# Optimization experiments

Hardware: AMD Instinct MI355X
Metric: run time of the kernel (lower is better)

The kernel has to match this reference:

```python
import jax, jax.numpy as jnp
import numpy as np

B, L, D = 16, 64, 768
E, R, T = 100000, 200, 1000000
NUM_WAYS, NUM_STEPS = 2, 3


def setup_inputs() -> dict:
    key = jax.random.key(0)
    k = jax.random.split(key, 12)
    s = 0.02  # matches nn.init.normal_(std=0.02)
    return {
        "heads": jax.random.uniform(k[0], (B, E), dtype=jnp.float32),
        "q_embeddings": jax.random.normal(k[1], (B, D), dtype=jnp.float32),
        "q_word_h": jax.random.normal(k[2], (B, L, D), dtype=jnp.float32),
        "attention_mask": jnp.ones((B, L), dtype=jnp.int32),
        "entity_range": jnp.ones((B, E), dtype=jnp.float32),
        "subj": jax.random.randint(k[3], (T,), 0, E, dtype=jnp.int32),
        "rel": jax.random.randint(k[4], (T,), 0, R, dtype=jnp.int32),
        "obj": jax.random.randint(k[5], (T,), 0, E, dtype=jnp.int32),
        "rel_importance": jnp.ones((R,), dtype=jnp.float32),
        "entity_emb": jax.random.normal(k[6], (E, D), dtype=jnp.float32) * s,
        "match_w": jax.random.normal(k[7], (D, D), dtype=jnp.float32) * s,
        "match_b": jnp.zeros((D,), dtype=jnp.float32),
        "step_w": jax.random.normal(k[8], (NUM_WAYS * NUM_STEPS, D, D), dtype=jnp.float32) * s,
        "step_b": jnp.zeros((NUM_WAYS * NUM_STEPS, D), dtype=jnp.float32),
        "rel_w": jax.random.normal(k[9], (NUM_WAYS, D, R), dtype=jnp.float32) * s,
        "rel_b": jnp.zeros((NUM_WAYS, R), dtype=jnp.float32),
        "hop_w": jax.random.normal(k[10], (NUM_WAYS, D, NUM_STEPS), dtype=jnp.float32) * s,
        "hop_b": jnp.zeros((NUM_WAYS, NUM_STEPS), dtype=jnp.float32),
        "temperature": jnp.ones((1,), dtype=jnp.float32),
    }


def _safe_row_norm(x):
    s = jnp.sum(x, axis=1, keepdims=True)
    return x / jnp.where(s > 0, s, 1.0)


def reference(heads, q_embeddings, q_word_h, attention_mask, entity_range,
              subj, rel, obj, rel_importance, entity_emb, match_w, match_b,
              step_w, step_b, rel_w, rel_b, hop_w, hop_b, temperature):
    # follow(e, r): sparse.mm(Msubj, e.T) is a row-gather e[:, subj];
    # sparse.mm(Mrel, wr.T) is wr[:, rel]; Mobj.T @ x is scatter-add over obj.
    def follow(e, r):
        wr = r * rel_importance[None, :]                      # [B, R]
        x = jnp.take(e, subj, axis=1) * jnp.take(wr, rel, axis=1)  # [B, T]
        res = jnp.zeros_like(e).at[:, obj].add(x)             # [B, E]
        res = jnp.clip(res, 0.0, 1.0)
        m = jnp.max(res, axis=1, keepdims=True)
        return res / jnp.where(m > 0, m, 1.0)

    mask_f = attention_mask.astype(jnp.float32)
    d = q_embeddings.shape[-1]
    # direct entity matching (dropout = identity in eval)
    qem = q_embeddings @ match_w + match_b
    direct = jax.nn.sigmoid((qem @ entity_emb.T) / jnp.sqrt(jnp.float32(d)))
    enhanced = _safe_row_norm(heads * (1.0 + 0.3 * direct))

    e_score = jnp.zeros_like(heads)
    for w in range(NUM_WAYS):
        last_e = enhanced  # num_ways > 1 branch
        ent_probs = []
        for t in range(NUM_STEPS):
            i = w * NUM_STEPS + t
            cq = jnp.tanh(q_embeddings @ step_w[i] + step_b[i])       # [B, D]
            q_logits = jnp.einsum('bd,bld->bl', cq, q_word_h) / temperature
            q_dist = jax.nn.softmax(q_logits, axis=1) * mask_f
            q_dist = q_dist / (jnp.sum(q_dist, axis=1, keepdims=True) + 1e-6)
            ctx = jnp.einsum('bl,bld->bd', q_dist, q_word_h)          # [B, D]
            rel_dist = jax.nn.softmax(ctx @ rel_w[w] + rel_b[w], axis=-1)
            next_e = follow(last_e, rel_dist)
            if t > 0:
                next_e = 0.7 * next_e + 0.3 * last_e  # residual, res_weight=0.3
            last_e = _safe_row_norm(next_e * entity_range)
            ent_probs.append(last_e)
        hop_res = jnp.stack(ent_probs, axis=1)                        # [B, S, E]
        hop_attn = jax.nn.softmax(q_embeddings @ hop_w[w] + hop_b[w], axis=1)[:, :, None]
        way_e = jnp.sum(hop_res * hop_attn, axis=1)                   # [B, E]
        if w == 0:
            way_e = way_e * (1.0 + 0.15 * direct)  # final_direct_weight
        e_score = e_score + way_e
    return e_score
```

## Files before the change

### kernel.cpp

```cpp
#include <hip/hip_runtime.h>
#include <cstdint>

constexpr int kB = 16;
constexpr int kL = 64;
constexpr int kD = 768;
constexpr int kE = 100000;
constexpr int kR = 200;
constexpr int kT = 1000000;
constexpr size_t kEB = (size_t)kE * 16;
constexpr int kEBq = kE * 4;

__global__ void __launch_bounds__(256) k_init(const float* __restrict__ heads,
        const float* __restrict__ er, float* __restrict__ headsT, float* __restrict__ erT,
        float* __restrict__ escT, int* __restrict__ cnt, unsigned* __restrict__ rmax,
        float* __restrict__ ssum, float* __restrict__ hsum) {
    int tid = blockIdx.x * blockDim.x + threadIdx.x;
    int gsz = gridDim.x * blockDim.x;
    if (tid < 96) { rmax[tid] = 0u; ssum[tid] = 0.f; }
    if (tid < 16) hsum[tid] = 0.f;
    float4 z4 = make_float4(0.f, 0.f, 0.f, 0.f);
    float4* esc4 = (float4*)escT;
    for (int i = tid; i < kEBq; i += gsz) esc4[i] = z4;
    for (int i = tid; i < kE; i += gsz) cnt[i] = 0;
    const float4* h4 = (const float4*)heads;
    const float4* r4 = (const float4*)er;
    for (int q = tid; q < kE / 4; q += gsz) {
        float hv[16][4], rv[16][4];
#pragma unroll
        for (int b = 0; b < 16; b++) {
            float4 h = h4[b * (kE / 4) + q];
            float4 r = r4[b * (kE / 4) + q];
            hv[b][0] = h.x; hv[b][1] = h.y; hv[b][2] = h.z; hv[b][3] = h.w;
            rv[b][0] = r.x; rv[b][1] = r.y; rv[b][2] = r.z; rv[b][3] = r.w;
        }
        float4* oh = (float4*)headsT + (size_t)q * 16;
        float4* orr = (float4*)erT + (size_t)q * 16;
#pragma unroll
        for (int u = 0; u < 4; u++) {
#pragma unroll
            for (int c = 0; c < 4; c++) {
                oh[u * 4 + c] = make_float4(hv[4*c][u], hv[4*c+1][u], hv[4*c+2][u], hv[4*c+3][u]);
                orr[u * 4 + c] = make_float4(rv[4*c][u], rv[4*c+1][u], rv[4*c+2][u], rv[4*c+3][u]);
            }
        }
    }
}

__global__ void k_hist(const int* __restrict__ obj, int* __restrict__ cnt) {
    int i = blockIdx.x * blockDim.x + threadIdx.x;
    int st = gridDim.x * blockDim.x;
    for (; i < kT; i += st) atomicAdd(&cnt[obj[i]], 1);
}

__global__ void k_scan1(const int* __restrict__ cnt, int* __restrict__ row, int* __restrict__ bsum) {
    __shared__ int s[512];
    int o = blockIdx.x * 512 + threadIdx.x;
    int v = (o < kE) ? cnt[o] : 0;
    s[threadIdx.x] = v;
    __syncthreads();
    for (int off = 1; off < 512; off <<= 1) {
        int t = (threadIdx.x >= off) ? s[threadIdx.x - off] : 0;
        __syncthreads();
        s[threadIdx.x] += t;
        __syncthreads();
    }
    if (o < kE) row[o + 1] = s[threadIdx.x];
    if (threadIdx.x == 511) bsum[blockIdx.x] = s[511];
}

__global__ void k_scan2(int* __restrict__ bsum, int nb) {
    __shared__ int s[256];
    int t = threadIdx.x;
    int v = (t < nb) ? bsum[t] : 0;
    s[t] = v;
    __syncthreads();
    for (int off = 1; off < 256; off <<= 1) {
        int x = (t >= off) ? s[t - off] : 0;
        __syncthreads();
        s[t] += x;
        __syncthreads();
    }
    if (t < nb) bsum[t] = s[t] - v;
}

__global__ void k_scan3(const int* __restrict__ cnt, int* __restrict__ row,
                        int* __restrict__ fill, const int* __restrict__ bsum) {
    int o = blockIdx.x * blockDim.x + threadIdx.x;
    if (o == 0) row[0] = 0;
    if (o < kE) {
        int incl = row[o + 1] + bsum[o / 512];
        row[o + 1] = incl;
        fill[o] = incl - cnt[o];
    }
}

__global__ void k_scatter(const int* __restrict__ subj, const int* __restrict__ rel,
                          const int* __restrict__ obj, int* __restrict__ fill,
                          int2* __restrict__ sr) {
    int i = blockIdx.x * blockDim.x + threadIdx.x;
    int st = gridDim.x * blockDim.x;
    for (; i < kT; i += st) {
        int o = obj[i];
        int p = atomicAdd(&fill[o], 1);
        sr[p] = make_int2(subj[i], rel[i]);
    }
}

__global__ void __launch_bounds__(192) k_dense(const float* __restrict__ q,
        const float* __restrict__ mw, const float* __restrict__ mb,
        const float* __restrict__ sw, const float* __restrict__ sb,
        float* __restrict__ cq) {
    int tid = threadIdx.x;
    int b = blockIdx.x, i = blockIdx.y;
    const float* W    = (i == 0) ? mw : sw + (size_t)(i - 1) * kD * kD;
    const float* bias = (i == 0) ? mb : sb + (size_t)(i - 1) * kD;
    const float* qr   = q + (size_t)b * kD;
    const float4* W4 = (const float4*)W;
    float4 acc = ((const float4*)bias)[tid];
#pragma unroll 4
    for (int k = 0; k < kD; k++) {
        float qk = qr[k];
        float4 wv = W4[k * 192 + tid];
        acc.x += qk * wv.x; acc.y += qk * wv.y; acc.z += qk * wv.z; acc.w += qk * wv.w;
    }
    if (i > 0) { acc.x = tanhf(acc.x); acc.y = tanhf(acc.y); acc.z = tanhf(acc.z); acc.w = tanhf(acc.w); }
    ((float4*)cq)[((size_t)i * 16 + b) * 192 + tid] = acc;
}

__global__ void __launch_bounds__(192) k_hop(const float* __restrict__ q,
        const float* __restrict__ hw, const float* __restrict__ hb,
        float* __restrict__ hopL) {
    int w = blockIdx.x, b = blockIdx.y, t = threadIdx.x;
    __shared__ float red[3][192];
    const float4* q4 = (const float4*)(q + (size_t)b * kD);
    float4 qv = q4[t];
    const float* hp = hw + ((size_t)w * kD + 4 * t) * 3;
    float p[3];
#pragma unroll
    for (int s = 0; s < 3; s++)
        p[s] = qv.x * hp[s] + qv.y * hp[3 + s] + qv.z * hp[6 + s] + qv.w * hp[9 + s];
#pragma unroll
    for (int s = 0; s < 3; s++) red[s][t] = p[s];
    __syncthreads();
    for (int off = 96; off >= 3; off >>= 1) {
        if (t < off) {
#pragma unroll
            for (int s = 0; s < 3; s++) red[s][t] += red[s][t + off];
        }
        __syncthreads();
    }
    if (t == 0) {
        float lg[3];
#pragma unroll
        for (int s = 0; s < 3; s++) lg[s] = red[s][0] + red[s][1] + red[s][2] + hb[w * 3 + s];
        float mx = fmaxf(lg[0], fmaxf(lg[1], lg[2]));
        float e0 = expf(lg[0] - mx), e1 = expf(lg[1] - mx), e2 = expf(lg[2] - mx);
        float z = e0 + e1 + e2;
        hopL[(w * 3 + 0) * 16 + b] = e0 / z;
        hopL[(w * 3 + 1) * 16 + b] = e1 / z;
        hopL[(w * 3 + 2) * 16 + b] = e2 / z;
    }
}

__global__ void __launch_bounds__(256) k_ctx(const float* __restrict__ cq,
        const float* __restrict__ qwh, const int* __restrict__ mask,
        const float* __restrict__ rw, const float* __restrict__ rb,
        const float* __restrict__ rimp, const float* __restrict__ temp,
        float* __restrict__ wrT) {
    int i = blockIdx.x, b = blockIdx.y, w = i / 3;
    __shared__ float red[64][4];
    __shared__ float dist[64];
    __shared__ float ctx[768];
    __shared__ float rl[200];
    __shared__ float tbuf[8];
    int tid = threadIdx.x;
    const float4* c4 = (const float4*)(cq + ((size_t)(i + 1) * 16 + b) * kD);
    const float4* qh4 = (const float4*)(qwh + (size_t)b * kL * kD);
    {
        int l = tid >> 2, part = tid & 3;
        float a = 0.f;
        for (int u = 0; u < 48; u++) {
            float4 qv = qh4[l * 192 + part * 48 + u];
            float4 cv = c4[part * 48 + u];
            a += qv.x * cv.x + qv.y * cv.y + qv.z * cv.z + qv.w * cv.w;
        }
        red[l][part] = a;
    }
    __syncthreads();
    if (tid < 64) {
        float lg = (red[tid][0] + red[tid][1] + red[tid][2] + red[tid][3]) / temp[0];
        float mx = lg;
        for (int o = 32; o > 0; o >>= 1) mx = fmaxf(mx, __shfl_xor(mx, o));
        float e = expf(lg - mx);
        float z = e;
        for (int o = 32; o > 0; o >>= 1) z += __shfl_xor(z, o);
        float p = e / z * (float)mask[b * kL + tid];
        float s = p;
        for (int o = 32; o > 0; o >>= 1) s += __shfl_xor(s, o);
        dist[tid] = p / (s + 1e-6f);
    }
    __syncthreads();
    if (tid < 192) {
        float4 a = make_float4(0.f, 0.f, 0.f, 0.f);
        for (int l = 0; l < 64; l++) {
            float dl = dist[l];
            float4 qv = qh4[l * 192 + tid];
            a.x += dl * qv.x; a.y += dl * qv.y; a.z += dl * qv.z; a.w += dl * qv.w;
        }
        ((float4*)ctx)[tid] = a;
    }
    __syncthreads();
    if (tid < kR) {
        float a = rb[w * kR + tid];
        const float* Wr = rw + (size_t)w * kD * kR;
#pragma unroll 4
        for (int d = 0; d < kD; d++) a += ctx[d] * Wr[(size_t)d * kR + tid];
        rl[tid] = a;
    }
    __syncthreads();
    {
        float v = (tid < kR) ? rl[tid] : -1e30f;
        float mx = v;
        for (int o = 32; o > 0; o >>= 1) mx = fmaxf(mx, __shfl_xor(mx, o));
        if ((tid & 63) == 0) tbuf[tid >> 6] = mx;
        __syncthreads();
        mx = fmaxf(fmaxf(tbuf[0], tbuf[1]), fmaxf(tbuf[2], tbuf[3]));
        float e = expf(v - mx);
        float z = e;
        for (int o = 32; o > 0; o >>= 1) z += __shfl_xor(z, o);
        if ((tid & 63) == 0) tbuf[4 + (tid >> 6)] = z;
        __syncthreads();
        z = tbuf[4] + tbuf[5] + tbuf[6] + tbuf[7];
        if (tid < kR) wrT[((size_t)i * kR + tid) * 16 + b] = (e / z) * rimp[tid];
    }
}

__global__ void __launch_bounds__(256) k_direct(const float4* __restrict__ emb4,
        const float4* __restrict__ q4, const float4* __restrict__ headsT4,
        float4* __restrict__ directT4, float4* __restrict__ enhU4,
        float* __restrict__ hsum) {
    __shared__ float4 lds[256 * 13];
    __shared__ float hs[16];
    const int t = threadIdx.x;
    if (t < 16) hs[t] = 0.f;
    const int e0 = blockIdx.x * 128;
    const int ent = t & 127;
    const int half = t >> 7;
    float acc[16];
#pragma unroll
    for (int b = 0; b < 16; b++) acc[b] = 0.f;
    for (int c = 0; c < 8; c++) {
        __syncthreads();
#pragma unroll
        for (int u = 0; u < 12; u++) {
            int l = u * 256 + t;
            int seg = l / 12, part = l - seg * 12;
            int ph = ((seg & 1) << 7) | (seg >> 1);
            int ge = e0 + (seg >> 1);
            float4 v = make_float4(0.f, 0.f, 0.f, 0.f);
            if (ge < kE) v = emb4[(size_t)ge * 192 + (seg & 1) * 96 + c * 12 + part];
            lds[ph * 13 + part] = v;
        }
        __syncthreads();
#pragma unroll
        for (int j = 0; j < 12; j++) {
            float4 ev = lds[t * 13 + j];
            int qk = half * 96 + c * 12 + j;
#pragma unroll
            for (int b = 0; b < 16; b++) {
                float4 qv = q4[b * 192 + qk];
                acc[b] += ev.x * qv.x + ev.y * qv.y + ev.z * qv.z + ev.w * qv.w;
            }
        }
    }
    __syncthreads();
    float* red = (float*)lds;
    if (half == 1) {
#pragma unroll
        for (int b = 0; b < 16; b++) red[ent * 17 + b] = acc[b];
    }
    __syncthreads();
    if (half == 0) {
        int ge = e0 + ent;
        const float invs = 0.03608439182435161f;
        float v[16];
        if (ge < kE) {
            float d[16];
#pragma unroll
            for (int b = 0; b < 16; b++) {
                float x = acc[b] + red[ent * 17 + b];
                d[b] = 1.f / (1.f + expf(-x * invs));
            }
            float4 hq[4];
#pragma unroll
            for (int cc = 0; cc < 4; cc++) {
                directT4[(size_t)ge * 4 + cc] = make_float4(d[4*cc], d[4*cc+1], d[4*cc+2], d[4*cc+3]);
                hq[cc] = headsT4[(size_t)ge * 4 + cc];
            }
#pragma unroll
            for (int cc = 0; cc < 4; cc++) {
                float4 e;
                e.x = hq[cc].x * (1.f + 0.3f * d[4*cc+0]);
                e.y = hq[cc].y * (1.f + 0.3f * d[4*cc+1]);
                e.z = hq[cc].z * (1.f + 0.3f * d[4*cc+2]);
                e.w = hq[cc].w * (1.f + 0.3f * d[4*cc+3]);
                enhU4[(size_t)ge * 4 + cc] = e;
                v[4*cc+0] = e.x; v[4*cc+1] = e.y; v[4*cc+2] = e.z; v[4*cc+3] = e.w;
            }
        } else {
#pragma unroll
            for (int b = 0; b < 16; b++) v[b] = 0.f;
        }
#pragma unroll
        for (int b = 0; b < 16; b++) {
            float s = v[b];
            for (int o = 32; o > 0; o >>= 1) s += __shfl_xor(s, o);
            if ((t & 63) == 0) atomicAdd(&hs[b], s);
        }
    }
    __syncthreads();
    if (t < 16) atomicAdd(&hsum[t], hs[t]);
}

__global__ void __launch_bounds__(256) k_follow(const float4* __restrict__ srcU4,
        const float4* __restrict__ wrT4, const int* __restrict__ row,
        const int2* __restrict__ sr, float4* __restrict__ resOut4,
        unsigned* __restrict__ rmax, const float* __restrict__ rowsum,
        const float4* __restrict__ Un4, const float* __restrict__ nssum,
        const float4* __restrict__ nhc4, const float4* __restrict__ directT4,
        float4* __restrict__ escT4, int do_acc, int nscale) {
    __shared__ float4 wrs[kR * 4];
    __shared__ unsigned umax[16];
    int tid = threadIdx.x;
    if (tid < 16) umax[tid] = 0u;
    {
        const float4* rs4 = (const float4*)rowsum;
        for (int idx = tid; idx < kR * 4; idx += 256) {
            float4 s = rs4[idx & 3];
            float4 wv = wrT4[idx];
            wv.x *= (s.x > 0.f) ? 1.f / s.x : 1.f;
            wv.y *= (s.y > 0.f) ? 1.f / s.y : 1.f;
            wv.z *= (s.z > 0.f) ? 1.f / s.z : 1.f;
            wv.w *= (s.w > 0.f) ? 1.f / s.w : 1.f;
            wrs[idx] = wv;
        }
    }
    __syncthreads();
    int slot = (blockIdx.x * 256 + tid) >> 2;
    int bc = tid & 3;
    float4 a = make_float4(0.f, 0.f, 0.f, 0.f);
    if (slot < kE) {
        int f = slot * 4 + bc;
        if (do_acc) {
            float4 sv = ((const float4*)nssum)[bc];
            float4 si;
            si.x = (sv.x > 0.f) ? 1.f / sv.x : 1.f;
            si.y = (sv.y > 0.f) ? 1.f / sv.y : 1.f;
            si.z = (sv.z > 0.f) ? 1.f / sv.z : 1.f;
            si.w = (sv.w > 0.f) ? 1.f / sv.w : 1.f;
            float4 u = Un4[f];
            float4 hc = nhc4[bc];
            float4 e = escT4[f];
            if (nscale) {
                float4 d = directT4[f];
                e.x += hc.x * u.x * si.x * (1.f + 0.15f * d.x);
                e.y += hc.y * u.y * si.y * (1.f + 0.15f * d.y);
                e.z += hc.z * u.z * si.z * (1.f + 0.15f * d.z);
                e.w += hc.w * u.w * si.w * (1.f + 0.15f * d.w);
            } else {
                e.x += hc.x * u.x * si.x;
                e.y += hc.y * u.y * si.y;
                e.z += hc.z * u.z * si.z;
                e.w += hc.w * u.w * si.w;
            }
            escT4[f] = e;
        }
        int j0 = row[slot], j1 = row[slot + 1];
        float4 a2 = make_float4(0.f, 0.f, 0.f, 0.f);
        int j = j0;
        for (; j + 2 <= j1; j += 2) {
            int2 p0 = sr[j], p1 = sr[j + 1];
            float4 s0 = srcU4[p0.x * 4 + bc];
            float4 w0 = wrs[p0.y * 4 + bc];
            float4 s1 = srcU4[p1.x * 4 + bc];
            float4 w1 = wrs[p1.y * 4 + bc];
            a.x += s0.x * w0.x; a.y += s0.y * w0.y; a.z += s0.z * w0.z; a.w += s0.w * w0.w;
            a2.x += s1.x * w1.x; a2.y += s1.y * w1.y; a2.z += s1.z * w1.z; a2.w += s1.w * w1.w;
        }
        if (j < j1) {
            int2 p = sr[j];
            float4 s0 = srcU4[p.x * 4 + bc];
            float4 w0 = wrs[p.y * 4 + bc];
            a.x += s0.x * w0.x; a.y += s0.y * w0.y; a.z += s0.z * w0.z; a.w += s0.w * w0.w;
        }
        a.x = fminf(fmaxf(a.x + a2.x, 0.f), 1.f);
        a.y = fminf(fmaxf(a.y + a2.y, 0.f), 1.f);
        a.z = fminf(fmaxf(a.z + a2.z, 0.f), 1.f);
        a.w = fminf(fmaxf(a.w + a2.w, 0.f), 1.f);
        resOut4[f] = a;
    }
    for (int o = 4; o < 64; o <<= 1) {
        a.x = fmaxf(a.x, __shfl_xor(a.x, o));
        a.y = fmaxf(a.y, __shfl_xor(a.y, o));
        a.z = fmaxf(a.z, __shfl_xor(a.z, o));
        a.w = fmaxf(a.w, __shfl_xor(a.w, o));
    }
    if ((tid & 63) < 4) {
        atomicMax(&umax[bc * 4 + 0], __float_as_uint(a.x));
        atomicMax(&umax[bc * 4 + 1], __float_as_uint(a.y));
        atomicMax(&umax[bc * 4 + 2], __float_as_uint(a.z));
        atomicMax(&umax[bc * 4 + 3], __float_as_uint(a.w));
    }
    __syncthreads();
    if (tid < 16) atomicMax(&rmax[tid], umax[tid]);
}

__global__ void __launch_bounds__(256) k_combine(float4* __restrict__ res4,
        const float4* __restrict__ uprev4, const float* __restrict__ ssum_prev,
        const float4* __restrict__ erT4, const unsigned* __restrict__ rmax16,
        float* __restrict__ ssum_out, int has_res) {
    __shared__ float ls[16];
    int tid = threadIdx.x;
    if (tid < 16) ls[tid] = 0.f;
    __syncthreads();
    int bc = tid & 3;
    uint4 rm = ((const uint4*)rmax16)[bc];
    float4 mi;
    { float m;
      m = __uint_as_float(rm.x); mi.x = (m > 0.f) ? 1.f / m : 1.f;
      m = __uint_as_float(rm.y); mi.y = (m > 0.f) ? 1.f / m : 1.f;
      m = __uint_as_float(rm.z); mi.z = (m > 0.f) ? 1.f / m : 1.f;
      m = __uint_as_float(rm.w); mi.w = (m > 0.f) ? 1.f / m : 1.f; }
    float4 si = make_float4(1.f, 1.f, 1.f, 1.f);
    if (has_res) {
        float4 s = ((const float4*)ssum_prev)[bc];
        si.x = (s.x > 0.f) ? 1.f / s.x : 1.f;
        si.y = (s.y > 0.f) ? 1.f / s.y : 1.f;
        si.z = (s.z > 0.f) ? 1.f / s.z : 1.f;
        si.w = (s.w > 0.f) ? 1.f / s.w : 1.f;
    }
    float4 su = make_float4(0.f, 0.f, 0.f, 0.f);
    int gsz = gridDim.x * 256;
    for (int f = blockIdx.x * 256 + tid; f < kEBq; f += gsz) {
        float4 v = res4[f];
        v.x *= mi.x; v.y *= mi.y; v.z *= mi.z; v.w *= mi.w;
        if (has_res) {
            float4 u = uprev4[f];
            v.x = 0.7f * v.x + 0.3f * u.x * si.x;
            v.y = 0.7f * v.y + 0.3f * u.y * si.y;
            v.z = 0.7f * v.z + 0.3f * u.z * si.z;
            v.w = 0.7f * v.w + 0.3f * u.w * si.w;
        }
        float4 er = erT4[f];
        v.x *= er.x; v.y *= er.y; v.z *= er.z; v.w *= er.w;
        res4[f] = v;
        su.x += v.x; su.y += v.y; su.z += v.z; su.w += v.w;
    }
    for (int o = 4; o < 64; o <<= 1) {
        su.x += __shfl_xor(su.x, o);
        su.y += __shfl_xor(su.y, o);
        su.z += __shfl_xor(su.z, o);
        su.w += __shfl_xor(su.w, o);
    }
    if ((tid & 63) < 4) {
        atomicAdd(&ls[bc * 4 + 0], su.x);
        atomicAdd(&ls[bc * 4 + 1], su.y);
        atomicAdd(&ls[bc * 4 + 2], su.z);
        atomicAdd(&ls[bc * 4 + 3], su.w);
    }
    __syncthreads();
    if (tid < 16) atomicAdd(&ssum_out[tid], ls[tid]);
}

__global__ void k_final(const float4* __restrict__ escT4, const float4* __restrict__ U4,
                        const float* __restrict__ ssum5, const float* __restrict__ hc5,
                        float* __restrict__ out) {
    int e = blockIdx.x * blockDim.x + threadIdx.x;
    if (e >= kE) return;
    float val[16];
#pragma unroll
    for (int c = 0; c < 4; c++) {
        float4 es = escT4[(size_t)e * 4 + c];
        float4 u  = U4[(size_t)e * 4 + c];
        float4 s  = ((const float4*)ssum5)[c];
        float4 h  = ((const float4*)hc5)[c];
        float4 si;
        si.x = (s.x > 0.f) ? 1.f / s.x : 1.f;
        si.y = (s.y > 0.f) ? 1.f / s.y : 1.f;
        si.z = (s.z > 0.f) ? 1.f / s.z : 1.f;
        si.w = (s.w > 0.f) ? 1.f / s.w : 1.f;
        val[4*c+0] = es.x + h.x * u.x * si.x;
        val[4*c+1] = es.y + h.y * u.y * si.y;
        val[4*c+2] = es.z + h.z * u.z * si.z;
        val[4*c+3] = es.w + h.w * u.w * si.w;
    }
#pragma unroll
    for (int b = 0; b < 16; b++) out[(size_t)b * kE + e] = val[b];
}

extern "C" void kernel_launch(void* const* d_in, const int* in_sizes, int n_in,
                              void* d_out, int out_size, void* d_ws, size_t ws_size,
                              hipStream_t stream) {
    const float* heads   = (const float*)d_in[0];
    const float* qemb    = (const float*)d_in[1];
    const float* qwh     = (const float*)d_in[2];
    const int*   amask   = (const int*)d_in[3];
    const float* erange  = (const float*)d_in[4];
    const int*   subj    = (const int*)d_in[5];
    const int*   rel     = (const int*)d_in[6];
    const int*   obj     = (const int*)d_in[7];
    const float* rimp    = (const float*)d_in[8];
    const float* emb     = (const float*)d_in[9];
    const float* mw      = (const float*)d_in[10];
    const float* mb      = (const float*)d_in[11];
    const float* sw      = (const float*)d_in[12];
    const float* sb      = (const float*)d_in[13];
    const float* rw      = (const float*)d_in[14];
    const float* rb      = (const float*)d_in[15];
    const float* hw      = (const float*)d_in[16];
    const float* hb      = (const float*)d_in[17];
    const float* temp    = (const float*)d_in[18];
    float* out = (float*)d_out;

    float* base = (float*)d_ws;
    float* directT = base;
    float* headsT  = directT + kEB;
    float* erT     = headsT + kEB;
    float* enhU    = erT + kEB;
    float* U0      = enhU + kEB;
    float* U1      = U0 + kEB;
    float* escT    = U1 + kEB;
    float* cq      = escT + kEB;
    float* wrT     = cq + (size_t)7 * 16 * kD;
    float* hopL    = wrT + (size_t)6 * kR * 16;
    float* hsum    = hopL + 96;
    float* ssum    = hsum + 16;
    unsigned* rmax = (unsigned*)(ssum + 96);
    int* cnt       = (int*)(rmax + 96);
    int* row       = cnt + kE;
    int* fill      = row + kE + 1;
    int* bsum      = fill + kE;
    int2* sr = (int2*)(((uintptr_t)(bsum + 256) + 255) & ~(uintptr_t)255);
    float* Ubuf[2] = {U0, U1};

    k_init<<<512, 256, 0, stream>>>(heads, erange, headsT, erT, escT, cnt, rmax, ssum, hsum);
    k_hist<<<512, 256, 0, stream>>>(obj, cnt);
    const int nb = (kE + 511) / 512;
    k_scan1<<<nb, 512, 0, stream>>>(cnt, row, bsum);
    k_scan2<<<1, 256, 0, stream>>>(bsum, nb);
    k_scan3<<<(kE + 255) / 256, 256, 0, stream>>>(cnt, row, fill, bsum);
    k_scatter<<<512, 256, 0, stream>>>(subj, rel, obj, fill, sr);

    k_dense<<<dim3(16, 7), 192, 0, stream>>>(qemb, mw, mb, sw, sb, cq);
    k_hop<<<dim3(2, 16), 192, 0, stream>>>(qemb, hw, hb, hopL);
    k_ctx<<<dim3(6, 16), 256, 0, stream>>>(cq, qwh, amask, rw, rb, rimp, temp, wrT);

    k_direct<<<782, 256, 0, stream>>>((const float4*)emb, (const float4*)cq,
                                      (const float4*)headsT, (float4*)directT,
                                      (float4*)enhU, hsum);

    for (int i = 0; i < 6; i++) {
        int w = i / 3, t = i % 3;
        const float* srcU = (t == 0) ? enhU : Ubuf[(i - 1) & 1];
        const float* rowsum = (t == 0) ? hsum : ssum + (i - 1) * 16;
        int do_acc = (i > 0);
        const float* Un = do_acc ? Ubuf[(i - 1) & 1] : enhU;
        const float* nss = do_acc ? ssum + (i - 1) * 16 : hsum;
        const float* nhc = hopL + (do_acc ? (i - 1) * 16 : 0);
        int nscale = do_acc ? ((i - 1) < 3 ? 1 : 0) : 0;
        k_follow<<<1563, 256, 0, stream>>>((const float4*)srcU,
                (const float4*)(wrT + (size_t)i * kR * 16), row, sr,
                (float4*)Ubuf[i & 1], rmax + i * 16, rowsum,
                (const float4*)Un, nss, (const float4*)nhc,
                (const float4*)directT, (float4*)escT, do_acc, nscale);
        k_combine<<<1024, 256, 0, stream>>>((float4*)Ubuf[i & 1],
                (const float4*)(t > 0 ? Ubuf[(i - 1) & 1] : enhU),
                t > 0 ? ssum + (i - 1) * 16 : hsum,
                (const float4*)erT, rmax + i * 16, ssum + i * 16, t > 0 ? 1 : 0);
        (void)w;
    }
    k_final<<<(kE + 255) / 256, 256, 0, stream>>>((const float4*)escT,
            (const float4*)Ubuf[1], ssum + 80, hopL + 80, out);
}
```

Measured before the change: 1.453 ms.

## Retile direct-score kernel, fold scan2 into scan3, widen follow gather unroll

The direct-score kernel now handles 64 entities per block, with four wavefronts each reducing a quarter of the feature dimension before a shared-memory cross-wave reduction. This doubles the grid and adds occupancy hints. The separate block-sum scan kernel is folded into the final scan kernel, which saves one launch at the cost of every block redundantly scanning the block sums. The CSR gather loop in the follow kernel now unrolls by four with int4 loads of (subj, rel) pairs and four accumulators, to expose more memory-level parallelism.

```diff
diff --git a/kernel.cpp b/kernel.cpp
--- a/kernel.cpp
+++ b/kernel.cpp
@@ -68,9 +68,11 @@
     if (threadIdx.x == 511) bsum[blockIdx.x] = s[511];
 }
 
-__global__ void k_scan2(int* __restrict__ bsum, int nb) {
+__global__ void k_scan3(const int* __restrict__ cnt, int* __restrict__ row,
+                        int* __restrict__ fill, const int* __restrict__ bsum) {
     __shared__ int s[256];
     int t = threadIdx.x;
+    const int nb = (kE + 511) / 512;
     int v = (t < nb) ? bsum[t] : 0;
     s[t] = v;
     __syncthreads();
@@ -80,15 +82,12 @@
         s[t] += x;
         __syncthreads();
     }
-    if (t < nb) bsum[t] = s[t] - v;
-}
-
-__global__ void k_scan3(const int* __restrict__ cnt, int* __restrict__ row,
-                        int* __restrict__ fill, const int* __restrict__ bsum) {
-    int o = blockIdx.x * blockDim.x + threadIdx.x;
+    int o = blockIdx.x * 256 + t;
     if (o == 0) row[0] = 0;
     if (o < kE) {
-        int incl = row[o + 1] + bsum[o / 512];
+        int blk = o / 512;
+        int pre = (blk == 0) ? 0 : s[blk - 1];
+        int incl = row[o + 1] + pre;
         row[o + 1] = incl;
         fill[o] = incl - cnt[o];
     }
@@ -235,91 +234,85 @@
     }
 }
 
-__global__ void __launch_bounds__(256) k_direct(const float4* __restrict__ emb4,
+__global__ void __launch_bounds__(256, 4) k_direct(const float4* __restrict__ emb4,
         const float4* __restrict__ q4, const float4* __restrict__ headsT4,
         float4* __restrict__ directT4, float4* __restrict__ enhU4,
         float* __restrict__ hsum) {
-    __shared__ float4 lds[256 * 13];
-    __shared__ float hs[16];
+    __shared__ float4 tile[64 * 25];
     const int t = threadIdx.x;
-    if (t < 16) hs[t] = 0.f;
-    const int e0 = blockIdx.x * 128;
-    const int ent = t & 127;
-    const int half = t >> 7;
+    const int l = t & 63;
+    const int wu = __builtin_amdgcn_readfirstlane(t >> 6);
+    const int e0 = blockIdx.x * 64;
     float acc[16];
 #pragma unroll
     for (int b = 0; b < 16; b++) acc[b] = 0.f;
+
     for (int c = 0; c < 8; c++) {
         __syncthreads();
 #pragma unroll
-        for (int u = 0; u < 12; u++) {
-            int l = u * 256 + t;
-            int seg = l / 12, part = l - seg * 12;
-            int ph = ((seg & 1) << 7) | (seg >> 1);
-            int ge = e0 + (seg >> 1);
+        for (int i = 0; i < 6; i++) {
+            int idx = i * 256 + t;
+            int r = idx / 24, col = idx - r * 24;
+            int ge = e0 + r;
             float4 v = make_float4(0.f, 0.f, 0.f, 0.f);
-            if (ge < kE) v = emb4[(size_t)ge * 192 + (seg & 1) * 96 + c * 12 + part];
-            lds[ph * 13 + part] = v;
-        }
-        __syncthreads();
-#pragma unroll
-        for (int j = 0; j < 12; j++) {
-            float4 ev = lds[t * 13 + j];
-            int qk = half * 96 + c * 12 + j;
+            if (ge < kE) v = emb4[(size_t)ge * 192 + c * 24 + col];
+            tile[r * 25 + col] = v;
+        }
+        __syncthreads();
+#pragma unroll
+        for (int j = 0; j < 6; j++) {
+            float4 ev = tile[l * 25 + wu * 6 + j];
+            int kq = c * 24 + wu * 6 + j;
 #pragma unroll
             for (int b = 0; b < 16; b++) {
-                float4 qv = q4[b * 192 + qk];
+                float4 qv = q4[b * 192 + kq];
                 acc[b] += ev.x * qv.x + ev.y * qv.y + ev.z * qv.z + ev.w * qv.w;
             }
         }
     }
     __syncthreads();
-    float* red = (float*)lds;
-    if (half == 1) {
-#pragma unroll
-        for (int b = 0; b < 16; b++) red[ent * 17 + b] = acc[b];
-    }
-    __syncthreads();
-    if (half == 0) {
-        int ge = e0 + ent;
-        const float invs = 0.03608439182435161f;
-        float v[16];
-        if (ge < kE) {
-            float d[16];
-#pragma unroll
-            for (int b = 0; b < 16; b++) {
-                float x = acc[b] + red[ent * 17 + b];
-                d[b] = 1.f / (1.f + expf(-x * invs));
-            }
-            float4 hq[4];
-#pragma unroll
-            for (int cc = 0; cc < 4; cc++) {
-                directT4[(size_t)ge * 4 + cc] = make_float4(d[4*cc], d[4*cc+1], d[4*cc+2], d[4*cc+3]);
-                hq[cc] = headsT4[(size_t)ge * 4 + cc];
-            }
-#pragma unroll
-            for (int cc = 0; cc < 4; cc++) {
-                float4 e;
-                e.x = hq[cc].x * (1.f + 0.3f * d[4*cc+0]);
-                e.y = hq[cc].y * (1.f + 0.3f * d[4*cc+1]);
-                e.z = hq[cc].z * (1.f + 0.3f * d[4*cc+2]);
-                e.w = hq[cc].w * (1.f + 0.3f * d[4*cc+3]);
-                enhU4[(size_t)ge * 4 + cc] = e;
-                v[4*cc+0] = e.x; v[4*cc+1] = e.y; v[4*cc+2] = e.z; v[4*cc+3] = e.w;
-            }
-        } else {
-#pragma unroll
-            for (int b = 0; b < 16; b++) v[b] = 0.f;
-        }
-#pragma unroll
-        for (int b = 0; b < 16; b++) {
-            float s = v[b];
-            for (int o = 32; o > 0; o >>= 1) s += __shfl_xor(s, o);
-            if ((t & 63) == 0) atomicAdd(&hs[b], s);
-        }
-    }
-    __syncthreads();
-    if (t < 16) atomicAdd(&hsum[t], hs[t]);
+    float* red = (float*)tile;
+    float4* red4 = (float4*)tile;
+#pragma unroll
+    for (int c4 = 0; c4 < 4; c4++)
+        red4[((wu * 64 + l) * 5) + c4] = make_float4(acc[c4*4], acc[c4*4+1], acc[c4*4+2], acc[c4*4+3]);
+    __syncthreads();
+    const int bq = t >> 6;
+    const int r = t & 63;
+    const int ge = e0 + r;
+    const float invs = 0.03608439182435161f;
+    float4 enh = make_float4(0.f, 0.f, 0.f, 0.f);
+    if (ge < kE) {
+        float d[4];
+#pragma unroll
+        for (int bb = 0; bb < 4; bb++) {
+            float x = 0.f;
+#pragma unroll
+            for (int w2 = 0; w2 < 4; w2++) x += red[(w2 * 64 + r) * 20 + bq * 4 + bb];
+            d[bb] = 1.f / (1.f + expf(-x * invs));
+        }
+        directT4[(size_t)ge * 4 + bq] = make_float4(d[0], d[1], d[2], d[3]);
+        float4 hq = headsT4[(size_t)ge * 4 + bq];
+        enh.x = hq.x * (1.f + 0.3f * d[0]);
+        enh.y = hq.y * (1.f + 0.3f * d[1]);
+        enh.z = hq.z * (1.f + 0.3f * d[2]);
+        enh.w = hq.w * (1.f + 0.3f * d[3]);
+        enhU4[(size_t)ge * 4 + bq] = enh;
+    }
+    float4 s = enh;
+#pragma unroll
+    for (int o = 1; o < 64; o <<= 1) {
+        s.x += __shfl_xor(s.x, o);
+        s.y += __shfl_xor(s.y, o);
+        s.z += __shfl_xor(s.z, o);
+        s.w += __shfl_xor(s.w, o);
+    }
+    if (l == 0) {
+        atomicAdd(&hsum[bq * 4 + 0], s.x);
+        atomicAdd(&hsum[bq * 4 + 1], s.y);
+        atomicAdd(&hsum[bq * 4 + 2], s.z);
+        atomicAdd(&hsum[bq * 4 + 3], s.w);
+    }
 }
 
 __global__ void __launch_bounds__(256) k_follow(const float4* __restrict__ srcU4,
@@ -348,7 +341,7 @@
     __syncthreads();
     int slot = (blockIdx.x * 256 + tid) >> 2;
     int bc = tid & 3;
-    float4 a = make_float4(0.f, 0.f, 0.f, 0.f);
+    float4 res = make_float4(0.f, 0.f, 0.f, 0.f);
     if (slot < kE) {
         int f = slot * 4 + bc;
         if (do_acc) {
@@ -376,40 +369,67 @@
             escT4[f] = e;
         }
         int j0 = row[slot], j1 = row[slot + 1];
+        float4 a0 = make_float4(0.f, 0.f, 0.f, 0.f);
+        float4 a1 = make_float4(0.f, 0.f, 0.f, 0.f);
         float4 a2 = make_float4(0.f, 0.f, 0.f, 0.f);
+        float4 a3 = make_float4(0.f, 0.f, 0.f, 0.f);
         int j = j0;
-        for (; j + 2 <= j1; j += 2) {
-            int2 p0 = sr[j], p1 = sr[j + 1];
-            float4 s0 = srcU4[p0.x * 4 + bc];
-            float4 w0 = wrs[p0.y * 4 + bc];
-            float4 s1 = srcU4[p1.x * 4 + bc];
-            float4 w1 = wrs[p1.y * 4 + bc];
-            a.x += s0.x * w0.x; a.y += s0.y * w0.y; a.z += s0.z * w0.z; a.w += s0.w * w0.w;
-            a2.x += s1.x * w1.x; a2.y += s1.y * w1.y; a2.z += s1.z * w1.z; a2.w += s1.w * w1.w;
+        if ((j & 1) && j < j1) {
+            int2 p = sr[j];
+            float4 s0 = srcU4[p.x * 4 + bc];
+            float4 w0 = wrs[p.y * 4 + bc];
+            a0.x += s0.x * w0.x; a0.y += s0.y * w0.y; a0.z += s0.z * w0.z; a0.w += s0.w * w0.w;
+            j++;
+        }
+        for (; j + 4 <= j1; j += 4) {
+            int4 p01 = *(const int4*)(sr + j);
+            int4 p23 = *(const int4*)(sr + j + 2);
+            float4 s0 = srcU4[p01.x * 4 + bc];
+            float4 s1 = srcU4[p01.z * 4 + bc];
+            float4 s2 = srcU4[p23.x * 4 + bc];
+            float4 s3 = srcU4[p23.z * 4 + bc];
+            float4 w0 = wrs[p01.y * 4 + bc];
+            float4 w1 = wrs[p01.w * 4 + bc];
+            float4 w2 = wrs[p23.y * 4 + bc];
+            float4 w3 = wrs[p23.w * 4 + bc];
+            a0.x += s0.x * w0.x; a0.y += s0.y * w0.y; a0.z += s0.z * w0.z; a0.w += s0.w * w0.w;
+            a1.x += s1.x * w1.x; a1.y += s1.y * w1.y; a1.z += s1.z * w1.z; a1.w += s1.w * w1.w;
+            a2.x += s2.x * w2.x; a2.y += s2.y * w2.y; a2.z += s2.z * w2.z; a2.w += s2.w * w2.w;
+            a3.x += s3.x * w3.x; a3.y += s3.y * w3.y; a3.z += s3.z * w3.z; a3.w += s3.w * w3.w;
+        }
+        if (j + 2 <= j1) {
+            int4 p01 = *(const int4*)(sr + j);
+            float4 s0 = srcU4[p01.x * 4 + bc];
+            float4 s1 = srcU4[p01.z * 4 + bc];
+            float4 w0 = wrs[p01.y * 4 + bc];
+            float4 w1 = wrs[p01.w * 4 + bc];
+            a0.x += s0.x * w0.x; a0.y += s0.y * w0.y; a0.z += s0.z * w0.z; a0.w += s0.w * w0.w;
+            a1.x += s1.x * w1.x; a1.y += s1.y * w1.y; a1.z += s1.z * w1.z; a1.w += s1.w * w1.w;
+            j += 2;
         }
         if (j < j1) {
             int2 p = sr[j];
             float4 s0 = srcU4[p.x * 4 + bc];
             float4 w0 = wrs[p.y * 4 + bc];
-            a.x += s0.x * w0.x; a.y += s0.y * w0.y; a.z += s0.z * w0.z; a.w += s0.w * w0.w;
-        }
-        a.x = fminf(fmaxf(a.x + a2.x, 0.f), 1.f);
-        a.y = fminf(fmaxf(a.y + a2.y, 0.f), 1.f);
-        a.z = fminf(fmaxf(a.z + a2.z, 0.f), 1.f);
-        a.w = fminf(fmaxf(a.w + a2.w, 0.f), 1.f);
-        resOut4[f] = a;
+            a2.x += s0.x * w0.x; a2.y += s0.y * w0.y; a2.z += s0.z * w0.z; a2.w += s0.w * w0.w;
+        }
+        res.x = fminf(fmaxf((a0.x + a1.x) + (a2.x + a3.x), 0.f), 1.f);
+        res.y = fminf(fmaxf((a0.y + a1.y) + (a2.y + a3.y), 0.f), 1.f);
+        res.z = fminf(fmaxf((a0.z + a1.z) + (a2.z + a3.z), 0.f), 1.f);
+        res.w = fminf(fmaxf((a0.w + a1.w) + (a2.w + a3.w), 0.f), 1.f);
+        resOut4[f] = res;
     }
     for (int o = 4; o < 64; o <<= 1) {
-        a.x = fmaxf(a.x, __shfl_xor(a.x, o));
-        a.y = fmaxf(a.y, __shfl_xor(a.y, o));
-        a.z = fmaxf(a.z, __shfl_xor(a.z, o));
-        a.w = fmaxf(a.w, __shfl_xor(a.w, o));
+        res.x = fmaxf(res.x, __shfl_xor(res.x, o));
+        res.y = fmaxf(res.y, __shfl_xor(res.y, o));
+        res.z = fmaxf(res.z, __shfl_xor(res.z, o));
+        res.w = fmaxf(res.w, __shfl_xor(res.w, o));
     }
     if ((tid & 63) < 4) {
-        atomicMax(&umax[bc * 4 + 0], __float_as_uint(a.x));
-        atomicMax(&umax[bc * 4 + 1], __float_as_uint(a.y));
-        atomicMax(&umax[bc * 4 + 2], __float_as_uint(a.z));
-        atomicMax(&umax[bc * 4 + 3], __float_as_uint(a.w));
+        atomicMax(&umax[bc * 4 + 0], __float_as_uint(res.x));
+        atomicMax(&umax[bc * 4 + 1], __float_as_uint(res.y));
+        atomicMax(&umax[bc * 4 + 2], __float_as_uint(res.z));
+        atomicMax(&umax[bc * 4 + 3], __float_as_uint(res.w));
     }
     __syncthreads();
     if (tid < 16) atomicMax(&rmax[tid], umax[tid]);
@@ -547,7 +567,6 @@
     k_hist<<<512, 256, 0, stream>>>(obj, cnt);
     const int nb = (kE + 511) / 512;
     k_scan1<<<nb, 512, 0, stream>>>(cnt, row, bsum);
-    k_scan2<<<1, 256, 0, stream>>>(bsum, nb);
     k_scan3<<<(kE + 255) / 256, 256, 0, stream>>>(cnt, row, fill, bsum);
     k_scatter<<<512, 256, 0, stream>>>(subj, rel, obj, fill, sr);
 
@@ -555,12 +574,12 @@
     k_hop<<<dim3(2, 16), 192, 0, stream>>>(qemb, hw, hb, hopL);
     k_ctx<<<dim3(6, 16), 256, 0, stream>>>(cq, qwh, amask, rw, rb, rimp, temp, wrT);
 
-    k_direct<<<782, 256, 0, stream>>>((const float4*)emb, (const float4*)cq,
-                                      (const float4*)headsT, (float4*)directT,
-                                      (float4*)enhU, hsum);
+    k_direct<<<1563, 256, 0, stream>>>((const float4*)emb, (const float4*)cq,
+                                       (const float4*)headsT, (float4*)directT,
+                                       (float4*)enhU, hsum);
 
     for (int i = 0; i < 6; i++) {
-        int w = i / 3, t = i % 3;
+        int t = i % 3;
         const float* srcU = (t == 0) ? enhU : Ubuf[(i - 1) & 1];
         const float* rowsum = (t == 0) ? hsum : ssum + (i - 1) * 16;
         int do_acc = (i > 0);
@@ -577,7 +596,6 @@
                 (const float4*)(t > 0 ? Ubuf[(i - 1) & 1] : enhU),
                 t > 0 ? ssum + (i - 1) * 16 : hsum,
                 (const float4*)erT, rmax + i * 16, ssum + i * 16, t > 0 ? 1 : 0);
-        (void)w;
     }
     k_final<<<(kE + 255) / 256, 256, 0, stream>>>((const float4*)escT,
             (const float4*)Ubuf[1], ssum + 80, hopL + 80, out);
```

Measured after the change: 1.453 ms. Within noise of the previous version (+0.0%).
